# Kernel tuning notes

Measured on AMD Instinct MI355X. Metric: run time of the kernel, lower is better.

Reference implementation:

```python
import jax, jax.numpy as jnp
import numpy as np

B, T, D = 2, 4096, 512
H = 8
HD = D // H


def setup_inputs() -> dict:
    key = jax.random.key(0)
    ks = jax.random.split(key, 6)
    s = 0.02
    return {
        "token_embed": jax.random.normal(ks[0], (B, T, D), jnp.float32),
        "Wq": jax.random.normal(ks[1], (D, D), jnp.float32) * s,
        "Wk": jax.random.normal(ks[2], (D, D), jnp.float32) * s,
        "Wv": jax.random.normal(ks[3], (D, D), jnp.float32) * s,
        "Wo": jax.random.normal(ks[4], (D, D), jnp.float32) * s,
        "bo": jnp.zeros((D,), jnp.float32),
    }


def reference(token_embed, Wq, Wk, Wv, Wo, bo):
    b, t, d_in = token_embed.shape
    # QKV projections (Linear without bias): x @ W^T with W stored [d_out, d_in]
    q = jnp.einsum("btd,ed->bte", token_embed, Wq).reshape(b, t, H, HD).transpose(0, 2, 1, 3)
    k = jnp.einsum("btd,ed->bte", token_embed, Wk).reshape(b, t, H, HD).transpose(0, 2, 1, 3)
    v = jnp.einsum("btd,ed->bte", token_embed, Wv).reshape(b, t, H, HD).transpose(0, 2, 1, 3)
    # Scores [b, h, t, t] with causal mask applied before scaling (as in source)
    scores = jnp.einsum("bhqd,bhkd->bhqk", q, k)
    causal = jnp.tril(jnp.ones((t, t), bool))  # True = keep
    scores = jnp.where(causal, scores, -jnp.inf)
    attn = jax.nn.softmax(scores / jnp.sqrt(jnp.float32(HD)), axis=-1)
    # dropout p=0.0 -> identity
    ctx = jnp.einsum("bhqk,bhkd->bhqd", attn, v)
    ctx = ctx.transpose(0, 2, 1, 3).reshape(b, t, H * HD)
    return jnp.einsum("btd,ed->bte", ctx, Wo) + bo
```

## Files before the change

### kernel.cpp

```cpp
#include <hip/hip_runtime.h>

#define B_  2
#define T_  4096
#define D_  512
#define H_  8
#define HD_ 64
#define M_  (B_*T_)

typedef _Float16 h16;
typedef _Float16 v8h __attribute__((ext_vector_type(8)));
typedef _Float16 h2  __attribute__((ext_vector_type(2)));
typedef float v4f __attribute__((ext_vector_type(4)));
typedef unsigned short us;

#define AS1 __attribute__((address_space(1)))
#define AS3 __attribute__((address_space(3)))

__device__ __forceinline__ float bf2f(us u){
  union { unsigned int i; float f; } v; v.i = ((unsigned int)u) << 16; return v.f;
}
__device__ __forceinline__ us f2bf(float f){
  union { float f; unsigned int u; } v; v.f = f;
  unsigned int r = v.u + 0x7FFFu + ((v.u >> 16) & 1u);
  return (us)(r >> 16);
}
__device__ __forceinline__ v4f zero4(){ v4f z; z[0]=0.f; z[1]=0.f; z[2]=0.f; z[3]=0.f; return z; }

__device__ __forceinline__ void glds16(const h16* g, h16* l){
  __builtin_amdgcn_global_load_lds((const AS1 int*)(const void*)g,
                                   (AS3 int*)(void*)l, 16, 0, 0);
}

__device__ __forceinline__ h2 pkrtz(float a, float b){
  auto t = __builtin_amdgcn_cvt_pkrtz(a, b);
  h2 r; __builtin_memcpy(&r, &t, sizeof(r)); return r;
}

__global__ __launch_bounds__(256) void conv_all(
    const void* __restrict__ x, const void* __restrict__ w0, const void* __restrict__ w1,
    const void* __restrict__ w2, const void* __restrict__ w3, const void* __restrict__ bo,
    h16* __restrict__ xb, h16* __restrict__ d0, h16* __restrict__ d1,
    h16* __restrict__ d2, h16* __restrict__ d3, float* __restrict__ bof)
{
  const int bid = blockIdx.x, tid = threadIdx.x;
  const void* src; int o0; int seg;
  h16* dst = nullptr;
  if (bid < 16384)      { src = x; o0 = bid * 256; dst = xb; seg = 0; }
  else if (bid < 20480) {
    const int wsel = (bid - 16384) >> 10;
    src = (wsel == 0) ? w0 : (wsel == 1) ? w1 : (wsel == 2) ? w2 : w3;
    dst = (wsel == 0) ? d0 : (wsel == 1) ? d1 : (wsel == 2) ? d2 : d3;
    o0 = ((bid - 16384) & 1023) * 256; seg = 0;
  } else                { src = bo; o0 = (bid - 20480) * 256; seg = 1; }

  __shared__ int sflag;
  if (tid == 0) sflag = 0;
  __syncthreads();
  const float probe = bf2f(((const us*)src)[o0 + tid]);
  if (!(fabsf(probe) < 1e4f)) atomicAdd(&sflag, 1);
  __syncthreads();
  const int isf32 = (sflag != 0);
  const int i = o0 + tid;
  const float v = isf32 ? ((const float*)src)[i] : bf2f(((const us*)src)[i]);
  if (seg) bof[i] = v;
  else     dst[i] = (h16)v;
}

__device__ __forceinline__ void stage4(const h16* __restrict__ A, const h16* __restrict__ W,
                                       int m0, int n0, int kk, h16* sA, h16* sB, int tid){
  const int colA = (tid & 3) << 3;
  const int rowT = tid >> 2;
#pragma unroll
  for (int rd = 0; rd < 2; rd++) {
    const int row = rd * 64 + rowT;
    const int f = rd * 2048 + tid * 8;
    glds16(A + (size_t)(m0 + row) * D_ + kk + colA, sA + f);
    glds16(W + (size_t)(n0 + row) * D_ + kk + colA, sB + f);
  }
}

__device__ __forceinline__ void gemm_core(const h16* __restrict__ A,
                                          const h16* __restrict__ W,
                                          int m0, int n0, h16* sA, h16* sB,
                                          v4f acc[4][4]) {
  const int tid = threadIdx.x;
  const int lane = tid & 63, wid = tid >> 6;
  const int r = lane & 15, q = lane >> 4;
#pragma unroll
  for (int i = 0; i < 4; i++)
#pragma unroll
    for (int j = 0; j < 4; j++) acc[i][j] = zero4();

  stage4(A, W, m0, n0, 0, sA, sB, tid);
#pragma unroll 1
  for (int kt = 0; kt < 16; kt++) {
    if (kt < 15) {
      const int nb = (kt + 1) & 1;
      stage4(A, W, m0, n0, (kt + 1) * 32, sA + nb * 4096, sB + nb * 4096, tid);
      asm volatile("s_waitcnt vmcnt(4)" ::: "memory");
    } else {
      asm volatile("s_waitcnt vmcnt(0)" ::: "memory");
    }
    asm volatile("s_barrier" ::: "memory");
    const h16* pA = sA + (kt & 1) * 4096 + ((wid & 1) * 64 + r) * 32 + q * 8;
    const h16* pB = sB + (kt & 1) * 4096 + ((wid >> 1) * 64 + r) * 32 + q * 8;
    v8h a[4], b[4];
#pragma unroll
    for (int i = 0; i < 4; i++) a[i] = *(const v8h*)(pA + i * 512);
#pragma unroll
    for (int j = 0; j < 4; j++) b[j] = *(const v8h*)(pB + j * 512);
#pragma unroll
    for (int i = 0; i < 4; i++)
#pragma unroll
      for (int j = 0; j < 4; j++)
        acc[i][j] = __builtin_amdgcn_mfma_f32_16x16x32_f16(a[i], b[j], acc[i][j], 0, 0, 0);
    asm volatile("s_barrier" ::: "memory");
  }
}

__global__ __launch_bounds__(256, 3) void gemm_qkv(
    const h16* __restrict__ X,
    const h16* __restrict__ Wq, const h16* __restrict__ Wk, const h16* __restrict__ Wv,
    h16* __restrict__ Qo, h16* __restrict__ Ko, h16* __restrict__ VTo)
{
  __shared__ h16 sA[2 * 4096], sB[2 * 4096];
  const h16* W = (blockIdx.z == 0) ? Wq : (blockIdx.z == 1 ? Wk : Wv);
  const int m0 = blockIdx.x * 128, n0 = blockIdx.y * 128;
  v4f acc[4][4];
  gemm_core(X, W, m0, n0, sA, sB, acc);
  const int lane = threadIdx.x & 63, wid = threadIdx.x >> 6;
  const int r = lane & 15, q = lane >> 4;
  const int wm = m0 + (wid & 1) * 64, wn = n0 + (wid >> 1) * 64;
  if (blockIdx.z == 2) {
#pragma unroll
    for (int i = 0; i < 4; i++)
#pragma unroll
      for (int j = 0; j < 4; j++)
#pragma unroll
        for (int rr = 0; rr < 4; rr++) {
          const int row = wm + i*16 + q*4 + rr;
          const int col = wn + j*16 + r;
          const int bb = row >> 12, tt = row & (T_ - 1);
          const int hh = col >> 6,  hd = col & 63;
          const int t6 = tt & 63;
          const int tperm = (tt & ~63) | (t6 & 3) | (((t6 >> 2) & 3) << 3)
                          | (((t6 >> 4) & 1) << 2) | (t6 & 32);
          VTo[((size_t)(((bb << 3) + hh) << 6) + hd) * T_ + tperm] = (h16)acc[i][j][rr];
        }
  } else {
    h16* Y = (blockIdx.z == 0) ? Qo : Ko;
    const float sc = (blockIdx.z == 0) ? 0.1803368801f : 1.0f;
#pragma unroll
    for (int i = 0; i < 4; i++)
#pragma unroll
      for (int j = 0; j < 4; j++)
#pragma unroll
        for (int rr = 0; rr < 4; rr++)
          Y[(size_t)(wm + i*16 + q*4 + rr) * D_ + wn + j*16 + r] = (h16)(acc[i][j][rr] * sc);
  }
}

__global__ __launch_bounds__(256, 3) void gemm_out(
    const h16* __restrict__ A, const h16* __restrict__ W,
    const float* __restrict__ bias, void* __restrict__ out, const void* __restrict__ xprobe)
{
  __shared__ h16 sA[2 * 4096], sB[2 * 4096];
  __shared__ int sflag;
  if (threadIdx.x == 0) sflag = 0;
  __syncthreads();
  const float probe = bf2f(((const us*)xprobe)[threadIdx.x]);
  if (!(fabsf(probe) < 1e4f)) atomicAdd(&sflag, 1);
  __syncthreads();
  const int flag = (sflag != 0);

  const int m0 = blockIdx.x * 128, n0 = blockIdx.y * 128;
  v4f acc[4][4];
  gemm_core(A, W, m0, n0, sA, sB, acc);
  const int lane = threadIdx.x & 63, wid = threadIdx.x >> 6;
  const int r = lane & 15, q = lane >> 4;
  const int wm = m0 + (wid & 1) * 64, wn = n0 + (wid >> 1) * 64;
#pragma unroll
  for (int i = 0; i < 4; i++)
#pragma unroll
    for (int j = 0; j < 4; j++)
#pragma unroll
      for (int rr = 0; rr < 4; rr++) {
        const int row = wm + i*16 + q*4 + rr;
        const int col = wn + j*16 + r;
        const float v = acc[i][j][rr] + bias[col];
        if (flag) ((float*)out)[(size_t)row * D_ + col] = v;
        else ((us*)out)[(size_t)row * D_ + col] = f2bf(v);
      }
}

__global__ __launch_bounds__(256, 4) void attn_kernel(
    const h16* __restrict__ Q, const h16* __restrict__ K,
    const h16* __restrict__ VT, h16* __restrict__ Ctx)
{
  const int h = blockIdx.x;
  const int pos = blockIdx.y + (blockIdx.z << 6);
  const int qc = 63 - (pos >> 1);
  const int b  = pos & 1;
  const int tid = threadIdx.x;
  const int wid = tid >> 6, lane = tid & 63;
  const int r = lane & 15, quad = lane >> 4;

  const size_t headoff = (size_t)b * T_ * D_ + (size_t)h * HD_;
  const h16* Qh  = Q + headoff;
  const h16* Kh  = K + headoff;
  const h16* VTh = VT + (size_t)(b * H_ + h) * HD_ * T_;
  h16* Ch = Ctx + headoff;

  __shared__ h16 sK[2][4096];
  __shared__ h16 sV[2][4096];

  const int qrow = qc * 64 + wid * 16;
  const int ntiles = qc + 1;

  const v8h aq0 = *(const v8h*)(Qh + (size_t)(qrow + r) * D_ + quad * 8);
  const v8h aq1 = *(const v8h*)(Qh + (size_t)(qrow + r) * D_ + 32 + quad * 8);

  v8h vone;
#pragma unroll
  for (int e = 0; e < 8; e++) vone[e] = (h16)1;

  v4f o[4];
#pragma unroll
  for (int j = 0; j < 4; j++) o[j] = zero4();
  v4f ol = zero4();

  const int srow = tid >> 3;
  const int sj = (tid & 7) ^ (srow & 7);
  const h16* kcur = Kh + (size_t)srow * D_ + sj * 8;
  const h16* vcur = VTh + (size_t)srow * T_ + sj * 8;
  h16* const dK0 = &sK[0][tid * 8], * const dK0b = &sK[0][2048 + tid * 8];
  h16* const dV0 = &sV[0][tid * 8], * const dV0b = &sV[0][2048 + tid * 8];
  h16* const dK1 = &sK[1][tid * 8], * const dK1b = &sK[1][2048 + tid * 8];
  h16* const dV1 = &sV[1][tid * 8], * const dV1b = &sV[1][2048 + tid * 8];

  glds16(kcur, dK0); glds16(kcur + 32 * D_, dK0b);
  glds16(vcur, dV0); glds16(vcur + 32 * T_, dV0b);
  kcur += 64 * D_; vcur += 64;

  const int xo0 = (quad ^ (r & 7)) * 8;
  const int xo1 = ((quad + 4) ^ (r & 7)) * 8;

#pragma unroll 1
  for (int kt = 0; kt < ntiles; kt++) {
    const h16* sKc = sK[kt & 1];
    const h16* sVc = sV[kt & 1];
    if (kt + 1 < ntiles) {
      if ((kt + 1) & 1) {
        glds16(kcur, dK1); glds16(kcur + 32 * D_, dK1b);
        glds16(vcur, dV1); glds16(vcur + 32 * T_, dV1b);
      } else {
        glds16(kcur, dK0); glds16(kcur + 32 * D_, dK0b);
        glds16(vcur, dV0); glds16(vcur + 32 * T_, dV0b);
      }
      kcur += 64 * D_; vcur += 64;
      asm volatile("s_waitcnt vmcnt(4)" ::: "memory");
    } else {
      asm volatile("s_waitcnt vmcnt(0)" ::: "memory");
    }
    asm volatile("s_barrier" ::: "memory");

    const h16* bK0 = sKc + r * 64 + xo0;
    const h16* bK1 = sKc + r * 64 + xo1;
    const h16* bV0 = sVc + r * 64 + xo0;
    const h16* bV1 = sVc + r * 64 + xo1;
    v8h ka[8], va[8];
#pragma unroll
    for (int kf = 0; kf < 4; kf++) {
      ka[2*kf]   = *(const v8h*)(bK0 + kf * 1024);
      ka[2*kf+1] = *(const v8h*)(bK1 + kf * 1024);
    }
#pragma unroll
    for (int j = 0; j < 4; j++) {
      va[2*j]   = *(const v8h*)(bV0 + j * 1024);
      va[2*j+1] = *(const v8h*)(bV1 + j * 1024);
    }
    v4f s_[4];
#pragma unroll
    for (int i = 0; i < 4; i++) {
      v4f t = zero4();
      t = __builtin_amdgcn_mfma_f32_16x16x32_f16(ka[2*i],   aq0, t, 0, 0, 0);
      t = __builtin_amdgcn_mfma_f32_16x16x32_f16(ka[2*i+1], aq1, t, 0, 0, 0);
      s_[i] = t;
    }
    const bool dg = (kt == ntiles - 1);
    union { v8h v; h2 p[4]; } pA, pB;
#pragma unroll
    for (int i = 0; i < 4; i++) {
      float e[4];
#pragma unroll
      for (int rr = 0; rr < 4; rr++) {
        float scv = s_[i][rr];
        if (dg) scv = (i * 16 + quad * 4 + rr <= wid * 16 + r) ? scv : -1e30f;
        e[rr] = exp2f(scv);
      }
      const h2 p01 = pkrtz(e[0], e[1]);
      const h2 p23 = pkrtz(e[2], e[3]);
      if (i < 2) { pA.p[i * 2] = p01; pA.p[i * 2 + 1] = p23; }
      else       { pB.p[(i - 2) * 2] = p01; pB.p[(i - 2) * 2 + 1] = p23; }
    }
    ol = __builtin_amdgcn_mfma_f32_16x16x32_f16(pA.v, vone, ol, 0, 0, 0);
    ol = __builtin_amdgcn_mfma_f32_16x16x32_f16(pB.v, vone, ol, 0, 0, 0);
#pragma unroll
    for (int j = 0; j < 4; j++) {
      o[j] = __builtin_amdgcn_mfma_f32_16x16x32_f16(pA.v, va[2*j],   o[j], 0, 0, 0);
      o[j] = __builtin_amdgcn_mfma_f32_16x16x32_f16(pB.v, va[2*j+1], o[j], 0, 0, 0);
    }
    asm volatile("s_barrier" ::: "memory");
  }
#pragma unroll
  for (int rr = 0; rr < 4; rr++) {
    const float inv = 1.0f / ol[rr];
    const size_t row = (size_t)(qrow + quad * 4 + rr) * D_;
#pragma unroll
    for (int j = 0; j < 4; j++)
      Ch[row + j * 16 + r] = (h16)(o[j][rr] * inv);
  }
}

extern "C" void kernel_launch(void* const* d_in, const int* in_sizes, int n_in,
                              void* d_out, int out_size, void* d_ws, size_t ws_size,
                              hipStream_t stream) {
  char* ws = (char*)d_ws;
  h16* xb  = (h16*)(ws + 0);
  h16* qb  = (h16*)(ws + 8388608);
  h16* kb  = (h16*)(ws + 16777216);
  h16* vt  = (h16*)(ws + 25165824);
  h16* ctx = (h16*)(ws + 33554432);
  h16* wqb = (h16*)(ws + 41943040);
  h16* wkb = (h16*)(ws + 41943040 + 524288);
  h16* wvb = (h16*)(ws + 41943040 + 2 * 524288);
  h16* wob = (h16*)(ws + 41943040 + 3 * 524288);
  float* bof = (float*)(ws + 41943040 + 4 * 524288);

  conv_all<<<20482, 256, 0, stream>>>(d_in[0], d_in[1], d_in[2], d_in[3], d_in[4],
                                      d_in[5], xb, wqb, wkb, wvb, wob, bof);
  gemm_qkv<<<dim3(M_ / 128, D_ / 128, 3), 256, 0, stream>>>(xb, wqb, wkb, wvb, qb, kb, vt);
  attn_kernel<<<dim3(H_, 64, B_), 256, 0, stream>>>(qb, kb, vt, ctx);
  gemm_out<<<dim3(M_ / 128, D_ / 128, 1), 256, 0, stream>>>(ctx, wob, bof, d_out, d_in[0]);
}
```

Baseline: 188.0 us.

## Load attention K/V fragments directly from global memory and split keys across waves

The attention kernel stops staging K and V tiles through LDS with barriers. Each wave now loads its MFMA fragments straight from global memory into registers, software-pipelined with double-buffered register fragments. The four waves are split into two query-row halves times two key halves, and partial outputs and row sums are combined through LDS at the end. The aim is to remove LDS traffic and per-tile barriers. In exchange, global and L2 load traffic goes up, register pressure rises (launch bounds drop to 3 blocks per SM), and a final cross-wave reduction is added.

```diff
diff --git a/kernel.cpp b/kernel.cpp
--- a/kernel.cpp
+++ b/kernel.cpp
@@ -35,6 +35,8 @@
   auto t = __builtin_amdgcn_cvt_pkrtz(a, b);
   h2 r; __builtin_memcpy(&r, &t, sizeof(r)); return r;
 }
+
+#define MFMA32 __builtin_amdgcn_mfma_f32_16x16x32_f16
 
 __global__ __launch_bounds__(256) void conv_all(
     const void* __restrict__ x, const void* __restrict__ w0, const void* __restrict__ w1,
@@ -113,7 +115,7 @@
     for (int i = 0; i < 4; i++)
 #pragma unroll
       for (int j = 0; j < 4; j++)
-        acc[i][j] = __builtin_amdgcn_mfma_f32_16x16x32_f16(a[i], b[j], acc[i][j], 0, 0, 0);
+        acc[i][j] = MFMA32(a[i], b[j], acc[i][j], 0, 0, 0);
     asm volatile("s_barrier" ::: "memory");
   }
 }
@@ -193,7 +195,10 @@
       }
 }
 
-__global__ __launch_bounds__(256, 4) void attn_kernel(
+struct KFrag { v8h a0, a1, b0, b1; };
+struct VFrag { v8h v[4]; };
+
+__global__ __launch_bounds__(256, 3) void attn_kernel(
     const h16* __restrict__ Q, const h16* __restrict__ K,
     const h16* __restrict__ VT, h16* __restrict__ Ctx)
 {
@@ -204,6 +209,7 @@
   const int tid = threadIdx.x;
   const int wid = tid >> 6, lane = tid & 63;
   const int r = lane & 15, quad = lane >> 4;
+  const int kw = wid & 1, qw = wid >> 1;
 
   const size_t headoff = (size_t)b * T_ * D_ + (size_t)h * HD_;
   const h16* Qh  = Q + headoff;
@@ -211,115 +217,135 @@
   const h16* VTh = VT + (size_t)(b * H_ + h) * HD_ * T_;
   h16* Ch = Ctx + headoff;
 
-  __shared__ h16 sK[2][4096];
-  __shared__ h16 sV[2][4096];
-
-  const int qrow = qc * 64 + wid * 16;
-  const int ntiles = qc + 1;
-
-  const v8h aq0 = *(const v8h*)(Qh + (size_t)(qrow + r) * D_ + quad * 8);
-  const v8h aq1 = *(const v8h*)(Qh + (size_t)(qrow + r) * D_ + 32 + quad * 8);
+  __shared__ float red[4288];
+
+  const int q0 = qc * 64 + qw * 32 + r;
+  const v8h aq00 = *(const v8h*)(Qh + (size_t)q0 * D_ + quad * 8);
+  const v8h aq01 = *(const v8h*)(Qh + (size_t)q0 * D_ + 32 + quad * 8);
+  const v8h aq10 = *(const v8h*)(Qh + (size_t)(q0 + 16) * D_ + quad * 8);
+  const v8h aq11 = *(const v8h*)(Qh + (size_t)(q0 + 16) * D_ + 32 + quad * 8);
 
   v8h vone;
 #pragma unroll
   for (int e = 0; e < 8; e++) vone[e] = (h16)1;
 
-  v4f o[4];
-#pragma unroll
-  for (int j = 0; j < 4; j++) o[j] = zero4();
-  v4f ol = zero4();
-
-  const int srow = tid >> 3;
-  const int sj = (tid & 7) ^ (srow & 7);
-  const h16* kcur = Kh + (size_t)srow * D_ + sj * 8;
-  const h16* vcur = VTh + (size_t)srow * T_ + sj * 8;
-  h16* const dK0 = &sK[0][tid * 8], * const dK0b = &sK[0][2048 + tid * 8];
-  h16* const dV0 = &sV[0][tid * 8], * const dV0b = &sV[0][2048 + tid * 8];
-  h16* const dK1 = &sK[1][tid * 8], * const dK1b = &sK[1][2048 + tid * 8];
-  h16* const dV1 = &sV[1][tid * 8], * const dV1b = &sV[1][2048 + tid * 8];
-
-  glds16(kcur, dK0); glds16(kcur + 32 * D_, dK0b);
-  glds16(vcur, dV0); glds16(vcur + 32 * T_, dV0b);
-  kcur += 64 * D_; vcur += 64;
-
-  const int xo0 = (quad ^ (r & 7)) * 8;
-  const int xo1 = ((quad + 4) ^ (r & 7)) * 8;
-
-#pragma unroll 1
-  for (int kt = 0; kt < ntiles; kt++) {
-    const h16* sKc = sK[kt & 1];
-    const h16* sVc = sV[kt & 1];
-    if (kt + 1 < ntiles) {
-      if ((kt + 1) & 1) {
-        glds16(kcur, dK1); glds16(kcur + 32 * D_, dK1b);
-        glds16(vcur, dV1); glds16(vcur + 32 * T_, dV1b);
-      } else {
-        glds16(kcur, dK0); glds16(kcur + 32 * D_, dK0b);
-        glds16(vcur, dV0); glds16(vcur + 32 * T_, dV0b);
+  v4f o0[4], o1[4];
+#pragma unroll
+  for (int j = 0; j < 4; j++) { o0[j] = zero4(); o1[j] = zero4(); }
+  v4f ld0 = zero4(), ld1 = zero4();
+
+  const h16* kbase = Kh + (size_t)(kw * 32 + r) * D_ + quad * 8;
+  const h16* vbase = VTh + (size_t)r * T_ + kw * 32 + quad * 8;
+  const int kloc = kw * 32 + quad * 4;
+  const int qlim0 = qw * 32 + r, qlim1 = qw * 32 + 16 + r;
+
+#define ISSUEK(F, KT) do {                                                     \
+    const h16* kp_ = kbase + (size_t)(KT) * (64 * D_);                         \
+    F.a0 = *(const v8h*)(kp_);                                                 \
+    F.a1 = *(const v8h*)(kp_ + 32);                                            \
+    F.b0 = *(const v8h*)(kp_ + 16 * D_);                                       \
+    F.b1 = *(const v8h*)(kp_ + 16 * D_ + 32);                                  \
+  } while(0)
+
+#define ISSUEV(V, KT) do {                                                     \
+    const h16* vp_ = vbase + (size_t)(KT) * 64;                                \
+    _Pragma("unroll")                                                          \
+    for (int hdb_ = 0; hdb_ < 4; hdb_++)                                       \
+      V.v[hdb_] = *(const v8h*)(vp_ + (size_t)hdb_ * 16 * T_);                 \
+  } while(0)
+
+#define PQB(SA, SB, QLIM, PAU, MASKED) do {                                    \
+    float e_[8];                                                               \
+    _Pragma("unroll")                                                          \
+    for (int rr = 0; rr < 4; rr++) {                                           \
+      float v0_ = SA[rr], v1_ = SB[rr];                                        \
+      if (MASKED) {                                                            \
+        if (kloc + rr > (QLIM)) v0_ = -1e30f;                                  \
+        if (kloc + 16 + rr > (QLIM)) v1_ = -1e30f;                             \
+      }                                                                        \
+      e_[rr] = exp2f(v0_); e_[4 + rr] = exp2f(v1_);                            \
+    }                                                                          \
+    PAU.p[0] = pkrtz(e_[0], e_[1]); PAU.p[1] = pkrtz(e_[2], e_[3]);            \
+    PAU.p[2] = pkrtz(e_[4], e_[5]); PAU.p[3] = pkrtz(e_[6], e_[7]);            \
+  } while(0)
+
+#define BODY(F, V, MASKED) do {                                                \
+    v4f s00 = zero4(), s01 = zero4(), s10 = zero4(), s11 = zero4();            \
+    s00 = MFMA32(F.a0, aq00, s00, 0,0,0); s00 = MFMA32(F.a1, aq01, s00, 0,0,0);\
+    s01 = MFMA32(F.a0, aq10, s01, 0,0,0); s01 = MFMA32(F.a1, aq11, s01, 0,0,0);\
+    s10 = MFMA32(F.b0, aq00, s10, 0,0,0); s10 = MFMA32(F.b1, aq01, s10, 0,0,0);\
+    s11 = MFMA32(F.b0, aq10, s11, 0,0,0); s11 = MFMA32(F.b1, aq11, s11, 0,0,0);\
+    union { v8h v; h2 p[4]; } pa0, pa1;                                        \
+    PQB(s00, s10, qlim0, pa0, MASKED);                                         \
+    PQB(s01, s11, qlim1, pa1, MASKED);                                         \
+    ld0 = MFMA32(pa0.v, vone, ld0, 0,0,0);                                     \
+    ld1 = MFMA32(pa1.v, vone, ld1, 0,0,0);                                     \
+    _Pragma("unroll")                                                          \
+    for (int hdb_ = 0; hdb_ < 4; hdb_++) {                                     \
+      o0[hdb_] = MFMA32(pa0.v, V.v[hdb_], o0[hdb_], 0,0,0);                    \
+      o1[hdb_] = MFMA32(pa1.v, V.v[hdb_], o1[hdb_], 0,0,0);                    \
+    }                                                                          \
+  } while(0)
+
+  KFrag fA, fB;
+  VFrag vx, vy;
+  ISSUEK(fA, 0);
+  const int nm = qc;
+  int kt = 0;
+  while (kt + 2 <= nm) {
+    ISSUEV(vx, kt);     ISSUEK(fB, kt + 1); BODY(fA, vx, false);
+    ISSUEV(vy, kt + 1); ISSUEK(fA, kt + 2); BODY(fB, vy, false);
+    kt += 2;
+  }
+  if (kt < nm) {
+    ISSUEV(vx, kt); ISSUEK(fB, kt + 1); BODY(fA, vx, false);
+    ISSUEV(vy, nm); BODY(fB, vy, true);
+  } else {
+    ISSUEV(vx, nm); BODY(fA, vx, true);
+  }
+
+  float* seg = red + qw * 2112;
+  float* lred = red + 4224;
+  if (kw) {
+#pragma unroll
+    for (int hdb = 0; hdb < 4; hdb++)
+#pragma unroll
+      for (int j = 0; j < 4; j++) {
+        seg[(quad * 4 + j) * 66 + hdb * 16 + r] = o0[hdb][j];
+        seg[(16 + quad * 4 + j) * 66 + hdb * 16 + r] = o1[hdb][j];
       }
-      kcur += 64 * D_; vcur += 64;
-      asm volatile("s_waitcnt vmcnt(4)" ::: "memory");
-    } else {
-      asm volatile("s_waitcnt vmcnt(0)" ::: "memory");
+    if (r == 0) {
+#pragma unroll
+      for (int j = 0; j < 4; j++) {
+        lred[qw * 32 + quad * 4 + j] = ld0[j];
+        lred[qw * 32 + 16 + quad * 4 + j] = ld1[j];
+      }
     }
-    asm volatile("s_barrier" ::: "memory");
-
-    const h16* bK0 = sKc + r * 64 + xo0;
-    const h16* bK1 = sKc + r * 64 + xo1;
-    const h16* bV0 = sVc + r * 64 + xo0;
-    const h16* bV1 = sVc + r * 64 + xo1;
-    v8h ka[8], va[8];
-#pragma unroll
-    for (int kf = 0; kf < 4; kf++) {
-      ka[2*kf]   = *(const v8h*)(bK0 + kf * 1024);
-      ka[2*kf+1] = *(const v8h*)(bK1 + kf * 1024);
+  }
+  __syncthreads();
+  if (!kw) {
+    float inv0[4], inv1[4];
+#pragma unroll
+    for (int j = 0; j < 4; j++) {
+      inv0[j] = 1.0f / (ld0[j] + lred[qw * 32 + quad * 4 + j]);
+      inv1[j] = 1.0f / (ld1[j] + lred[qw * 32 + 16 + quad * 4 + j]);
     }
 #pragma unroll
-    for (int j = 0; j < 4; j++) {
-      va[2*j]   = *(const v8h*)(bV0 + j * 1024);
-      va[2*j+1] = *(const v8h*)(bV1 + j * 1024);
-    }
-    v4f s_[4];
-#pragma unroll
-    for (int i = 0; i < 4; i++) {
-      v4f t = zero4();
-      t = __builtin_amdgcn_mfma_f32_16x16x32_f16(ka[2*i],   aq0, t, 0, 0, 0);
-      t = __builtin_amdgcn_mfma_f32_16x16x32_f16(ka[2*i+1], aq1, t, 0, 0, 0);
-      s_[i] = t;
-    }
-    const bool dg = (kt == ntiles - 1);
-    union { v8h v; h2 p[4]; } pA, pB;
-#pragma unroll
-    for (int i = 0; i < 4; i++) {
-      float e[4];
-#pragma unroll
-      for (int rr = 0; rr < 4; rr++) {
-        float scv = s_[i][rr];
-        if (dg) scv = (i * 16 + quad * 4 + rr <= wid * 16 + r) ? scv : -1e30f;
-        e[rr] = exp2f(scv);
+    for (int hdb = 0; hdb < 4; hdb++)
+#pragma unroll
+      for (int j = 0; j < 4; j++) {
+        const float a0 = o0[hdb][j] + seg[(quad * 4 + j) * 66 + hdb * 16 + r];
+        const float a1 = o1[hdb][j] + seg[(16 + quad * 4 + j) * 66 + hdb * 16 + r];
+        Ch[(size_t)(qc * 64 + qw * 32 + quad * 4 + j) * D_ + hdb * 16 + r] =
+            (h16)(a0 * inv0[j]);
+        Ch[(size_t)(qc * 64 + qw * 32 + 16 + quad * 4 + j) * D_ + hdb * 16 + r] =
+            (h16)(a1 * inv1[j]);
       }
-      const h2 p01 = pkrtz(e[0], e[1]);
-      const h2 p23 = pkrtz(e[2], e[3]);
-      if (i < 2) { pA.p[i * 2] = p01; pA.p[i * 2 + 1] = p23; }
-      else       { pB.p[(i - 2) * 2] = p01; pB.p[(i - 2) * 2 + 1] = p23; }
-    }
-    ol = __builtin_amdgcn_mfma_f32_16x16x32_f16(pA.v, vone, ol, 0, 0, 0);
-    ol = __builtin_amdgcn_mfma_f32_16x16x32_f16(pB.v, vone, ol, 0, 0, 0);
-#pragma unroll
-    for (int j = 0; j < 4; j++) {
-      o[j] = __builtin_amdgcn_mfma_f32_16x16x32_f16(pA.v, va[2*j],   o[j], 0, 0, 0);
-      o[j] = __builtin_amdgcn_mfma_f32_16x16x32_f16(pB.v, va[2*j+1], o[j], 0, 0, 0);
-    }
-    asm volatile("s_barrier" ::: "memory");
-  }
-#pragma unroll
-  for (int rr = 0; rr < 4; rr++) {
-    const float inv = 1.0f / ol[rr];
-    const size_t row = (size_t)(qrow + quad * 4 + rr) * D_;
-#pragma unroll
-    for (int j = 0; j < 4; j++)
-      Ch[row + j * 16 + r] = (h16)(o[j][rr] * inv);
-  }
+  }
+#undef ISSUEK
+#undef ISSUEV
+#undef PQB
+#undef BODY
 }
 
 extern "C" void kernel_launch(void* const* d_in, const int* in_sizes, int n_in,
```

New measurement: 251.3 us. +33.6%, slower.

## Split attention key tile across warp pairs with shared-memory cross-warp reduction

Applied to the files above, without the earlier changes.

Restructures the attention inner loop so each warp handles 32 query rows against half of each 64-key tile, instead of 16 query rows against the full tile. Each K/V fragment loaded from shared memory is now reused across two query sub-blocks, which cuts LDS reads per MFMA. Partial outputs and row sums are combined through shared memory in an epilogue. This adds two extra barriers and a reduction step, and raises accumulator register use per warp.

```diff
diff --git a/kernel.cpp b/kernel.cpp
--- a/kernel.cpp
+++ b/kernel.cpp
@@ -13,6 +13,8 @@
 typedef float v4f __attribute__((ext_vector_type(4)));
 typedef unsigned short us;
 
+union PaU { v8h v; h2 p[4]; };
+
 #define AS1 __attribute__((address_space(1)))
 #define AS3 __attribute__((address_space(3)))
 
@@ -35,6 +37,8 @@
   auto t = __builtin_amdgcn_cvt_pkrtz(a, b);
   h2 r; __builtin_memcpy(&r, &t, sizeof(r)); return r;
 }
+
+#define MFMA32 __builtin_amdgcn_mfma_f32_16x16x32_f16
 
 __global__ __launch_bounds__(256) void conv_all(
     const void* __restrict__ x, const void* __restrict__ w0, const void* __restrict__ w1,
@@ -113,7 +117,7 @@
     for (int i = 0; i < 4; i++)
 #pragma unroll
       for (int j = 0; j < 4; j++)
-        acc[i][j] = __builtin_amdgcn_mfma_f32_16x16x32_f16(a[i], b[j], acc[i][j], 0, 0, 0);
+        acc[i][j] = MFMA32(a[i], b[j], acc[i][j], 0, 0, 0);
     asm volatile("s_barrier" ::: "memory");
   }
 }
@@ -204,6 +208,7 @@
   const int tid = threadIdx.x;
   const int wid = tid >> 6, lane = tid & 63;
   const int r = lane & 15, quad = lane >> 4;
+  const int kw = wid & 1, qw = wid >> 1;
 
   const size_t headoff = (size_t)b * T_ * D_ + (size_t)h * HD_;
   const h16* Qh  = Q + headoff;
@@ -211,52 +216,52 @@
   const h16* VTh = VT + (size_t)(b * H_ + h) * HD_ * T_;
   h16* Ch = Ctx + headoff;
 
-  __shared__ h16 sK[2][4096];
-  __shared__ h16 sV[2][4096];
-
-  const int qrow = qc * 64 + wid * 16;
+  __shared__ h16 smem[4][4096];
+
+  const int q0 = qc * 64 + qw * 32;
   const int ntiles = qc + 1;
 
-  const v8h aq0 = *(const v8h*)(Qh + (size_t)(qrow + r) * D_ + quad * 8);
-  const v8h aq1 = *(const v8h*)(Qh + (size_t)(qrow + r) * D_ + 32 + quad * 8);
+  const v8h aq00 = *(const v8h*)(Qh + (size_t)(q0 + r) * D_ + quad * 8);
+  const v8h aq01 = *(const v8h*)(Qh + (size_t)(q0 + r) * D_ + 32 + quad * 8);
+  const v8h aq10 = *(const v8h*)(Qh + (size_t)(q0 + 16 + r) * D_ + quad * 8);
+  const v8h aq11 = *(const v8h*)(Qh + (size_t)(q0 + 16 + r) * D_ + 32 + quad * 8);
 
   v8h vone;
 #pragma unroll
   for (int e = 0; e < 8; e++) vone[e] = (h16)1;
 
-  v4f o[4];
-#pragma unroll
-  for (int j = 0; j < 4; j++) o[j] = zero4();
-  v4f ol = zero4();
+  v4f o0[4], o1[4];
+#pragma unroll
+  for (int j = 0; j < 4; j++) { o0[j] = zero4(); o1[j] = zero4(); }
+  v4f ld0 = zero4(), ld1 = zero4();
 
   const int srow = tid >> 3;
   const int sj = (tid & 7) ^ (srow & 7);
   const h16* kcur = Kh + (size_t)srow * D_ + sj * 8;
   const h16* vcur = VTh + (size_t)srow * T_ + sj * 8;
-  h16* const dK0 = &sK[0][tid * 8], * const dK0b = &sK[0][2048 + tid * 8];
-  h16* const dV0 = &sV[0][tid * 8], * const dV0b = &sV[0][2048 + tid * 8];
-  h16* const dK1 = &sK[1][tid * 8], * const dK1b = &sK[1][2048 + tid * 8];
-  h16* const dV1 = &sV[1][tid * 8], * const dV1b = &sV[1][2048 + tid * 8];
-
-  glds16(kcur, dK0); glds16(kcur + 32 * D_, dK0b);
-  glds16(vcur, dV0); glds16(vcur + 32 * T_, dV0b);
+
+  glds16(kcur, &smem[0][tid * 8]); glds16(kcur + 32 * D_, &smem[0][2048 + tid * 8]);
+  glds16(vcur, &smem[2][tid * 8]); glds16(vcur + 32 * T_, &smem[2][2048 + tid * 8]);
   kcur += 64 * D_; vcur += 64;
 
   const int xo0 = (quad ^ (r & 7)) * 8;
   const int xo1 = ((quad + 4) ^ (r & 7)) * 8;
+  const int xov = ((quad + kw * 4) ^ (r & 7)) * 8;
+  const int krow = kw * 32 + r;
+  const int kloc = kw * 32 + quad * 4;
+  const int qlim0 = qw * 32 + r, qlim1 = qw * 32 + 16 + r;
 
 #pragma unroll 1
   for (int kt = 0; kt < ntiles; kt++) {
-    const h16* sKc = sK[kt & 1];
-    const h16* sVc = sV[kt & 1];
+    const int cb = kt & 1;
+    const h16* sKc = smem[cb];
+    const h16* sVc = smem[2 + cb];
     if (kt + 1 < ntiles) {
-      if ((kt + 1) & 1) {
-        glds16(kcur, dK1); glds16(kcur + 32 * D_, dK1b);
-        glds16(vcur, dV1); glds16(vcur + 32 * T_, dV1b);
-      } else {
-        glds16(kcur, dK0); glds16(kcur + 32 * D_, dK0b);
-        glds16(vcur, dV0); glds16(vcur + 32 * T_, dV0b);
-      }
+      const int nb = (kt + 1) & 1;
+      glds16(kcur, &smem[nb][tid * 8]);
+      glds16(kcur + 32 * D_, &smem[nb][2048 + tid * 8]);
+      glds16(vcur, &smem[2 + nb][tid * 8]);
+      glds16(vcur + 32 * T_, &smem[2 + nb][2048 + tid * 8]);
       kcur += 64 * D_; vcur += 64;
       asm volatile("s_waitcnt vmcnt(4)" ::: "memory");
     } else {
@@ -264,61 +269,90 @@
     }
     asm volatile("s_barrier" ::: "memory");
 
-    const h16* bK0 = sKc + r * 64 + xo0;
-    const h16* bK1 = sKc + r * 64 + xo1;
-    const h16* bV0 = sVc + r * 64 + xo0;
-    const h16* bV1 = sVc + r * 64 + xo1;
-    v8h ka[8], va[8];
-#pragma unroll
-    for (int kf = 0; kf < 4; kf++) {
-      ka[2*kf]   = *(const v8h*)(bK0 + kf * 1024);
-      ka[2*kf+1] = *(const v8h*)(bK1 + kf * 1024);
-    }
+    const h16* bK = sKc + krow * 64;
+    const v8h ka0 = *(const v8h*)(bK + xo0);
+    const v8h ka1 = *(const v8h*)(bK + xo1);
+    const v8h ka2 = *(const v8h*)(bK + 16 * 64 + xo0);
+    const v8h ka3 = *(const v8h*)(bK + 16 * 64 + xo1);
+    v8h va[4];
+#pragma unroll
+    for (int j = 0; j < 4; j++)
+      va[j] = *(const v8h*)(sVc + (j * 16 + r) * 64 + xov);
+
+    v4f s00 = zero4(), s10 = zero4(), s01 = zero4(), s11 = zero4();
+    s00 = MFMA32(ka0, aq00, s00, 0,0,0); s00 = MFMA32(ka1, aq01, s00, 0,0,0);
+    s10 = MFMA32(ka2, aq00, s10, 0,0,0); s10 = MFMA32(ka3, aq01, s10, 0,0,0);
+    s01 = MFMA32(ka0, aq10, s01, 0,0,0); s01 = MFMA32(ka1, aq11, s01, 0,0,0);
+    s11 = MFMA32(ka2, aq10, s11, 0,0,0); s11 = MFMA32(ka3, aq11, s11, 0,0,0);
+
+    const bool dg = (kt == ntiles - 1);
+    PaU pa0, pa1;
+#pragma unroll
+    for (int qb = 0; qb < 2; qb++) {
+      const v4f& sa = qb ? s01 : s00;
+      const v4f& sb = qb ? s11 : s10;
+      const int qlim = qb ? qlim1 : qlim0;
+      float e0[4], e1[4];
+#pragma unroll
+      for (int rr = 0; rr < 4; rr++) {
+        float v0 = sa[rr], v1 = sb[rr];
+        if (dg) {
+          if (kloc + rr > qlim)      v0 = -1e30f;
+          if (kloc + 16 + rr > qlim) v1 = -1e30f;
+        }
+        e0[rr] = exp2f(v0); e1[rr] = exp2f(v1);
+      }
+      PaU* pa = qb ? &pa1 : &pa0;
+      pa->p[0] = pkrtz(e0[0], e0[1]); pa->p[1] = pkrtz(e0[2], e0[3]);
+      pa->p[2] = pkrtz(e1[0], e1[1]); pa->p[3] = pkrtz(e1[2], e1[3]);
+    }
+    ld0 = MFMA32(pa0.v, vone, ld0, 0,0,0);
+    ld1 = MFMA32(pa1.v, vone, ld1, 0,0,0);
 #pragma unroll
     for (int j = 0; j < 4; j++) {
-      va[2*j]   = *(const v8h*)(bV0 + j * 1024);
-      va[2*j+1] = *(const v8h*)(bV1 + j * 1024);
-    }
-    v4f s_[4];
-#pragma unroll
-    for (int i = 0; i < 4; i++) {
-      v4f t = zero4();
-      t = __builtin_amdgcn_mfma_f32_16x16x32_f16(ka[2*i],   aq0, t, 0, 0, 0);
-      t = __builtin_amdgcn_mfma_f32_16x16x32_f16(ka[2*i+1], aq1, t, 0, 0, 0);
-      s_[i] = t;
-    }
-    const bool dg = (kt == ntiles - 1);
-    union { v8h v; h2 p[4]; } pA, pB;
-#pragma unroll
-    for (int i = 0; i < 4; i++) {
-      float e[4];
-#pragma unroll
-      for (int rr = 0; rr < 4; rr++) {
-        float scv = s_[i][rr];
-        if (dg) scv = (i * 16 + quad * 4 + rr <= wid * 16 + r) ? scv : -1e30f;
-        e[rr] = exp2f(scv);
-      }
-      const h2 p01 = pkrtz(e[0], e[1]);
-      const h2 p23 = pkrtz(e[2], e[3]);
-      if (i < 2) { pA.p[i * 2] = p01; pA.p[i * 2 + 1] = p23; }
-      else       { pB.p[(i - 2) * 2] = p01; pB.p[(i - 2) * 2 + 1] = p23; }
-    }
-    ol = __builtin_amdgcn_mfma_f32_16x16x32_f16(pA.v, vone, ol, 0, 0, 0);
-    ol = __builtin_amdgcn_mfma_f32_16x16x32_f16(pB.v, vone, ol, 0, 0, 0);
+      o0[j] = MFMA32(pa0.v, va[j], o0[j], 0,0,0);
+      o1[j] = MFMA32(pa1.v, va[j], o1[j], 0,0,0);
+    }
+    asm volatile("s_barrier" ::: "memory");
+  }
+
+  __syncthreads();
+  float* const red = (float*)&smem[0][0];
+  float* const seg = red + qw * 2112;
+  float* const lred = red + 4224;
+  if (kw) {
+#pragma unroll
+    for (int hdb = 0; hdb < 4; hdb++)
+#pragma unroll
+      for (int j = 0; j < 4; j++) {
+        seg[(quad * 4 + j) * 66 + hdb * 16 + r] = o0[hdb][j];
+        seg[(16 + quad * 4 + j) * 66 + hdb * 16 + r] = o1[hdb][j];
+      }
+    if (r == 0) {
+#pragma unroll
+      for (int j = 0; j < 4; j++) {
+        lred[qw * 32 + quad * 4 + j] = ld0[j];
+        lred[qw * 32 + 16 + quad * 4 + j] = ld1[j];
+      }
+    }
+  }
+  __syncthreads();
+  if (!kw) {
+    float inv0[4], inv1[4];
 #pragma unroll
     for (int j = 0; j < 4; j++) {
-      o[j] = __builtin_amdgcn_mfma_f32_16x16x32_f16(pA.v, va[2*j],   o[j], 0, 0, 0);
-      o[j] = __builtin_amdgcn_mfma_f32_16x16x32_f16(pB.v, va[2*j+1], o[j], 0, 0, 0);
-    }
-    asm volatile("s_barrier" ::: "memory");
-  }
-#pragma unroll
-  for (int rr = 0; rr < 4; rr++) {
-    const float inv = 1.0f / ol[rr];
-    const size_t row = (size_t)(qrow + quad * 4 + rr) * D_;
-#pragma unroll
-    for (int j = 0; j < 4; j++)
-      Ch[row + j * 16 + r] = (h16)(o[j][rr] * inv);
+      inv0[j] = 1.0f / (ld0[j] + lred[qw * 32 + quad * 4 + j]);
+      inv1[j] = 1.0f / (ld1[j] + lred[qw * 32 + 16 + quad * 4 + j]);
+    }
+#pragma unroll
+    for (int hdb = 0; hdb < 4; hdb++)
+#pragma unroll
+      for (int j = 0; j < 4; j++) {
+        const float a0 = o0[hdb][j] + seg[(quad * 4 + j) * 66 + hdb * 16 + r];
+        const float a1 = o1[hdb][j] + seg[(16 + quad * 4 + j) * 66 + hdb * 16 + r];
+        Ch[(size_t)(q0 + quad * 4 + j) * D_ + hdb * 16 + r] = (h16)(a0 * inv0[j]);
+        Ch[(size_t)(q0 + 16 + quad * 4 + j) * D_ + hdb * 16 + r] = (h16)(a1 * inv1[j]);
+      }
   }
 }
 
```

Measured after the change: 179.8 us. 1.05x faster.
